# Kernel tuning notes

Hardware: AMD Instinct MI355X
Metric: run time of the kernel (lower is better)

Reference implementation:

```python
import jax, jax.numpy as jnp
import numpy as np

B, T, C_IN = 2, 4096, 1024
INTER, OUT = 1024, 1024
ROPE_DIM = 64
GAMMA = 0.99609375  # 1 - 2**-8
GROUPS = 32
EPS = 1e-6


def setup_inputs() -> dict:
    key = jax.random.key(0)
    k = jax.random.split(key, 4)
    return {
        "X_Q": jax.random.normal(k[0], (B, T, C_IN), dtype=jnp.float32),
        "W_Q": jax.random.normal(k[1], (C_IN, INTER), dtype=jnp.float32) / C_IN,
        "W_K": jax.random.normal(k[2], (C_IN, INTER), dtype=jnp.float32) / C_IN,
        "W_V": jax.random.normal(k[3], (C_IN, OUT), dtype=jnp.float32) / C_IN,
        "gn_weight": jnp.ones((OUT,), dtype=jnp.float32),
        "gn_bias": jnp.zeros((OUT,), dtype=jnp.float32),
    }


def _rope(x):
    # lucidrains RotaryEmbedding: rotate first ROPE_DIM features, pairwise-adjacent
    t = x.shape[-2]
    inv_freq = 1.0 / (10000.0 ** (jnp.arange(0, ROPE_DIM, 2, dtype=jnp.float32) / ROPE_DIM))
    freqs = jnp.arange(t, dtype=jnp.float32)[:, None] * inv_freq[None, :]  # [T, ROPE_DIM/2]
    freqs = jnp.repeat(freqs, 2, axis=-1)                                   # [T, ROPE_DIM]
    cos, sin = jnp.cos(freqs), jnp.sin(freqs)
    xr, xp = x[..., :ROPE_DIM], x[..., ROPE_DIM:]
    x1, x2 = xr[..., 0::2], xr[..., 1::2]
    rot = jnp.stack([-x2, x1], axis=-1).reshape(xr.shape)  # rotate_half (adjacent pairs)
    return jnp.concatenate([xr * cos + rot * sin, xp], axis=-1)


def _group_norm(x, w, b):
    # torch GroupNorm applied on x.reshape(-1, C)
    sh = x.shape
    c = sh[-1]
    xr = x.reshape(-1, GROUPS, c // GROUPS)
    mu = xr.mean(-1, keepdims=True)
    var = xr.var(-1, keepdims=True)
    xn = ((xr - mu) * jax.lax.rsqrt(var + EPS)).reshape(-1, c)
    return (xn * w + b).reshape(sh)


def reference(X_Q, W_Q, W_K, W_V, gn_weight, gn_bias):
    Q = jax.nn.silu(_rope(X_Q @ W_Q))  # [B,T,INTER]
    K = jax.nn.silu(_rope(X_Q @ W_K))
    V = jax.nn.silu(X_Q @ W_V)         # [B,T,OUT]
    A = jnp.einsum('btd,bsd->bts', Q, K)  # [B,T,T]
    # decay mask: original multiplies by _get_D(gamma,T).T -> gamma^(m-n) for m>=n
    n = jnp.arange(T)[:, None]
    m = jnp.arange(T)[None, :]
    upper = m >= n
    Dt = jnp.where(upper, GAMMA ** jnp.where(upper, m - n, 0).astype(jnp.float32), 0.0)
    A = A * Dt
    out = jnp.einsum('bts,bsd->btd', A, V)  # [B,T,OUT]
    # dropout p=0 (eval) -> identity
    return _group_norm(out, gn_weight, gn_bias)
```

## Files before the change

### kernel.cpp

```cpp
#include <hip/hip_runtime.h>


typedef __attribute__((ext_vector_type(8))) short bf16x8;
typedef __attribute__((ext_vector_type(4))) short bf16x4;
typedef __attribute__((ext_vector_type(4))) float f32x4;

#define MFMA16(a, b, c) __builtin_amdgcn_mfma_f32_16x16x32_bf16(a, b, c, 0, 0, 0)

static __device__ __forceinline__ short f2bf(float f) {
  unsigned u = __builtin_bit_cast(unsigned, f);
  u = (u + 0x7fffu + ((u >> 16) & 1u)) >> 16;
  return (short)u;
}

static __device__ __forceinline__ float fast_silu(float v) {
  return v * __builtin_amdgcn_rcpf(1.f + __expf(-v));
}

static __device__ __forceinline__ void gl_lds16(const void* g, void* l) {
  __builtin_amdgcn_global_load_lds(
      (const __attribute__((address_space(1))) void*)g,
      (__attribute__((address_space(3))) void*)l, 16, 0, 0);
}

static __device__ __forceinline__ int swzc(int col, int row) {
  return (((col >> 3) ^ (row & 7)) << 3) | (col & 7);
}

#define T_LEN 4096
#define CIN 1024

#define LOG2G (-0.0056465633f)
#define L2IF (0.41524101f)

__global__ __launch_bounds__(256)
void prep_kernel(const float* __restrict__ X, short* __restrict__ Xb,
                 const float* __restrict__ Wq, const float* __restrict__ Wk,
                 const float* __restrict__ Wv, short* __restrict__ WT) {
  __shared__ short tile[64][72];
  const int bx = blockIdx.x;
  const int tid = threadIdx.x;
  if (bx < 4096) {
    const int gid = bx * 256 + tid;
    const int row = gid >> 7;
    const int c = gid & 127;
    const float* s = &X[(size_t)gid * 8];
    float4 f0 = *(const float4*)s;
    float4 f1 = *(const float4*)(s + 4);
    bf16x8 v = {f2bf(f0.x), f2bf(f0.y), f2bf(f0.z), f2bf(f0.w),
                f2bf(f1.x), f2bf(f1.y), f2bf(f1.z), f2bf(f1.w)};
    const int pc = (c & 0x78) | ((c ^ row) & 7);
    *(bf16x8*)&Xb[(size_t)row * 1024 + pc * 8] = v;
    return;
  }
  const int bx2 = bx - 4096;
  const int k0 = (bx2 & 15) * 64, n0 = ((bx2 >> 4) & 15) * 64, mat = bx2 >> 8;
  const float* __restrict__ W = (mat == 0) ? Wq : (mat == 1) ? Wk : Wv;
  const int r = tid >> 4, c = tid & 15;
#pragma unroll
  for (int i = 0; i < 4; ++i) {
    int row = r + 16 * i;
    float4 f = *(const float4*)&W[(size_t)(k0 + row) * CIN + n0 + c * 4];
    tile[c * 4 + 0][row] = f2bf(f.x);
    tile[c * 4 + 1][row] = f2bf(f.y);
    tile[c * 4 + 2][row] = f2bf(f.z);
    tile[c * 4 + 3][row] = f2bf(f.w);
  }
  __syncthreads();
  const int n = tid >> 2, seg = tid & 3;
  bf16x8 lo = *(const bf16x8*)&tile[n][seg * 16];
  bf16x8 hi = *(const bf16x8*)&tile[n][seg * 16 + 8];
  const int R = mat * 1024 + n0 + n;
  const int a0 = (k0 >> 3) + seg * 2;
  short* base = &WT[(size_t)R * CIN];
  *(bf16x8*)&base[(a0 ^ (n & 7)) * 8] = lo;
  *(bf16x8*)&base[((a0 + 1) ^ (n & 7)) * 8] = hi;
}

#define GEMM_DECLS()                                   \
  const int tid = threadIdx.x;                         \
  const int lane = tid & 63, wave = tid >> 6;          \
  const int wm = wave >> 1, wn = wave & 1;             \
  const int l15 = lane & 15, quad = lane >> 4;         \
  const int srow = tid >> 3;                           \
  const int scol = (tid & 7) * 8;                      \
  const int asw = (l15 & 7);

#define ACC_INIT4(acc)                                 \
  _Pragma("unroll") for (int i = 0; i < 4; ++i)        \
  _Pragma("unroll") for (int j = 0; j < 4; ++j) {      \
    f32x4 z = {0.f, 0.f, 0.f, 0.f};                    \
    acc[i][j] = z;                                     \
  }

#define STAGE_TILE(dst, src, ld, r0, k0, nrows)        \
  _Pragma("unroll") for (int i = 0; i < (nrows) / 32; ++i) \
    gl_lds16(&src[(size_t)((r0) + i * 32 + srow) * (ld) + (k0) + scol], \
             &dst[i * 32 + srow][scol]);

#define FRAG_MFMA44(As, Bs, acc)                                            \
  {                                                                         \
    bf16x8 af[4][2], bfr[4][2];                                             \
    _Pragma("unroll") for (int im = 0; im < 4; ++im)                        \
    _Pragma("unroll") for (int ks = 0; ks < 2; ++ks)                        \
      af[im][ks] = *(const bf16x8*)&As[wm * 64 + im * 16 + l15]             \
                       [((ks * 4 + quad) ^ asw) * 8];                       \
    _Pragma("unroll") for (int in = 0; in < 4; ++in)                        \
    _Pragma("unroll") for (int ks = 0; ks < 2; ++ks)                        \
      bfr[in][ks] = *(const bf16x8*)&Bs[wn * 64 + in * 16 + l15]            \
                        [((ks * 4 + quad) ^ asw) * 8];                      \
    _Pragma("unroll") for (int ks = 0; ks < 2; ++ks)                        \
    _Pragma("unroll") for (int im = 0; im < 4; ++im)                        \
    _Pragma("unroll") for (int in = 0; in < 4; ++in)                        \
      acc[im][in] = MFMA16(af[im][ks], bfr[in][ks], acc[im][in]);           \
  }

__global__ __launch_bounds__(256, 2)
void qkv_gemm(const short* __restrict__ Xb, const short* __restrict__ WT,
              short* __restrict__ Qb, short* __restrict__ Kb,
              short* __restrict__ Vt) {
  __shared__ __align__(16) short As[128][64];
  __shared__ __align__(16) short Bs[128][64];
  GEMM_DECLS();
  const int m0 = blockIdx.x * 128;
  const int c0 = blockIdx.y * 128;

  f32x4 acc[4][4];
  ACC_INIT4(acc);

  for (int k0 = 0; k0 < CIN; k0 += 64) {
    __syncthreads();
    STAGE_TILE(As, Xb, CIN, m0, k0, 128);
    STAGE_TILE(Bs, WT, CIN, c0, k0, 128);
    __syncthreads();
    FRAG_MFMA44(As, Bs, acc);
  }

  const int mat = (c0 >> 10);
  const bool ropeBlk = (mat < 2) && ((c0 & 1023) == 0);
#pragma unroll
  for (int im = 0; im < 4; ++im) {
#pragma unroll
    for (int in = 0; in < 4; ++in) {
      const int c = c0 + wn * 64 + in * 16 + l15;
      const int colm = c & 1023;
      const int mbase = m0 + wm * 64 + im * 16 + quad * 4;
      short vv[4];
      if (ropeBlk && colm < 64) {
        const float invf = exp2f(-L2IF * (float)(colm >> 1));
#pragma unroll
        for (int r = 0; r < 4; ++r) {
          float v = acc[im][in][r];
          int t = (mbase + r) & (T_LEN - 1);
          float partner = __shfl_xor(v, 1, 64);
          float ang = (float)t * invf;
          float s_ = __sinf(ang), c_ = __cosf(ang);
          v = (colm & 1) ? (v * c_ + partner * s_) : (v * c_ - partner * s_);
          vv[r] = f2bf(fast_silu(v));
        }
      } else {
#pragma unroll
        for (int r = 0; r < 4; ++r) vv[r] = f2bf(fast_silu(acc[im][in][r]));
      }
      if (mat == 0) {
#pragma unroll
        for (int r = 0; r < 4; ++r)
          Qb[(size_t)(mbase + r) * 1024 + swzc(colm, mbase + r)] = vv[r];
      } else if (mat == 1) {
#pragma unroll
        for (int r = 0; r < 4; ++r)
          Kb[(size_t)(mbase + r) * 1024 + swzc(colm, mbase + r)] = vv[r];
      } else {
        bf16x4 v4 = {vv[0], vv[1], vv[2], vv[3]};
        *(bf16x4*)&Vt[(size_t)colm * 8192 +
                      (((mbase >> 3) ^ (colm & 7)) << 3) + (mbase & 7)] = v4;
      }
    }
  }
}

__global__ __launch_bounds__(256, 2)
void score_kernel(const short* __restrict__ Qb, const short* __restrict__ Kb,
                  short* __restrict__ Ab) {
  int idx = blockIdx.x;
  int ti = 0;
  while (idx >= 32 - ti) { idx -= 32 - ti; ++ti; }
  const int si = ti + idx;
  const int b = blockIdx.y;
  const int s0 = si * 128, t0 = ti * 128;

  __shared__ __align__(16) short Qs[128][64];
  __shared__ __align__(16) short Ks[128][64];
  GEMM_DECLS();

  f32x4 acc[4][4];
  ACC_INIT4(acc);

  for (int k0 = 0; k0 < 1024; k0 += 64) {
    __syncthreads();
    STAGE_TILE(Qs, Qb, 1024, b * T_LEN + t0, k0, 128);
    STAGE_TILE(Ks, Kb, 1024, b * T_LEN + s0, k0, 128);
    __syncthreads();
    FRAG_MFMA44(Qs, Ks, acc);
  }

#pragma unroll
  for (int im = 0; im < 4; ++im) {
#pragma unroll
    for (int in = 0; in < 4; ++in) {
      int s = s0 + wn * 64 + in * 16 + l15;
#pragma unroll
      for (int r = 0; r < 4; ++r) {
        int t = t0 + wm * 64 + im * 16 + quad * 4 + r;
        int d = s - t;
        float v = acc[im][in][r];
        v = (d < 0) ? 0.f : v * exp2f((float)d * LOG2G);
        Ab[((size_t)(b * T_LEN + t)) * T_LEN + swzc(s, t)] = f2bf(v);
      }
    }
  }
}

__global__ __launch_bounds__(256, 2)
void av_kernel(const short* __restrict__ Ab, const short* __restrict__ Vt,
               const float* __restrict__ gw, const float* __restrict__ gb,
               float* __restrict__ Out) {
  const int wgid = blockIdx.x;
  const int di = wgid & 7;
  const int q = (wgid >> 3) & 31;
  const int half = wgid >> 8;
  const int b = half;
  const int ti2 = half ? (31 - q) : q;
  const int t0 = ti2 * 128;
  const int n0 = di * 128;
  const int nIt = (T_LEN - t0) >> 6;

  __shared__ __align__(16) short As2[128][64];
  __shared__ __align__(16) short Vs[128][64];
  GEMM_DECLS();

  float w4[4], b4[4];
#pragma unroll
  for (int in = 0; in < 4; ++in) {
    int n = n0 + wn * 64 + in * 16 + l15;
    w4[in] = gw[n];
    b4[in] = gb[n];
  }

  f32x4 acc[4][4];
  ACC_INIT4(acc);

#pragma unroll 1
  for (int it = 0; it < nIt; ++it) {
    const int s = t0 + (it << 6);
    __syncthreads();
    STAGE_TILE(As2, Ab, T_LEN, b * T_LEN + t0, s, 128);
    STAGE_TILE(Vs, Vt, 8192, n0, b * T_LEN + s, 128);
    __syncthreads();
    FRAG_MFMA44(As2, Vs, acc);
  }

#pragma unroll
  for (int im = 0; im < 4; ++im) {
#pragma unroll
    for (int r = 0; r < 4; ++r) {
      int t = t0 + wm * 64 + im * 16 + quad * 4 + r;
      float* orow = &Out[((size_t)(b * T_LEN + t)) * 1024];
#pragma unroll
      for (int g = 0; g < 2; ++g) {
        float a0 = acc[im][g * 2][r], a1 = acc[im][g * 2 + 1][r];
        float s = a0 + a1;
        float qq = a0 * a0 + a1 * a1;
        s += __shfl_xor(s, 1, 64);
        qq += __shfl_xor(qq, 1, 64);
        s += __shfl_xor(s, 2, 64);
        qq += __shfl_xor(qq, 2, 64);
        s += __shfl_xor(s, 4, 64);
        qq += __shfl_xor(qq, 4, 64);
        s += __shfl_xor(s, 8, 64);
        qq += __shfl_xor(qq, 8, 64);
        float mean = s * (1.f / 32.f);
        float var = qq * (1.f / 32.f) - mean * mean;
        float rstd = rsqrtf(var + 1e-6f);
        int n = n0 + wn * 64 + g * 32 + l15;
        orow[n] = (a0 - mean) * rstd * w4[g * 2] + b4[g * 2];
        orow[n + 16] = (a1 - mean) * rstd * w4[g * 2 + 1] + b4[g * 2 + 1];
      }
    }
  }
}

extern "C" void kernel_launch(void* const* d_in, const int* in_sizes, int n_in,
                              void* d_out, int out_size, void* d_ws,
                              size_t ws_size, hipStream_t stream) {
  const float* X = (const float*)d_in[0];
  const float* Wq = (const float*)d_in[1];
  const float* Wk = (const float*)d_in[2];
  const float* Wv = (const float*)d_in[3];
  const float* gw = (const float*)d_in[4];
  const float* gb = (const float*)d_in[5];
  float* Out = (float*)d_out;

  short* Qb = (short*)d_ws;
  short* Kb = Qb + (size_t)8192 * 1024;
  short* Vt = Kb + (size_t)8192 * 1024;
  short* Ab = Vt + (size_t)8192 * 1024;
  short* Xb = Ab;
  short* WT = Xb + (size_t)8192 * 1024;

  prep_kernel<<<4864, 256, 0, stream>>>(X, Xb, Wq, Wk, Wv, WT);
  qkv_gemm<<<dim3(64, 24), 256, 0, stream>>>(Xb, WT, Qb, Kb, Vt);
  score_kernel<<<dim3(528, 2), 256, 0, stream>>>(Qb, Kb, Ab);
  av_kernel<<<512, 256, 0, stream>>>(Ab, Vt, gw, gb, Out);
}
```

Measured before the change: 280.9 us.

## Double-buffer QKV GEMM with async LDS prefetch and 256x128 tiles

The QKV projection GEMM now uses 512-thread blocks covering 256 rows by 128 columns, with two LDS buffers per operand. Direct global-to-LDS loads for the next K step are interleaved between MFMA phases, and s_setprio is raised around the MFMA bursts, replacing the old load-sync-compute loop. The aim is to hide global load latency behind matrix math and to reuse each B tile across more rows. In exchange LDS use doubles, there are more barriers per iteration, and the grid has half as many blocks, which may affect occupancy.

New measurement: 315.2 us. 1.12x slower.

```diff
diff --git a/kernel.cpp b/kernel.cpp
--- a/kernel.cpp
+++ b/kernel.cpp
@@ -115,26 +115,119 @@
       acc[im][in] = MFMA16(af[im][ks], bfr[in][ks], acc[im][in]);           \
   }
 
-__global__ __launch_bounds__(256, 2)
+__global__ __launch_bounds__(512, 2)
 void qkv_gemm(const short* __restrict__ Xb, const short* __restrict__ WT,
               short* __restrict__ Qb, short* __restrict__ Kb,
               short* __restrict__ Vt) {
-  __shared__ __align__(16) short As[128][64];
-  __shared__ __align__(16) short Bs[128][64];
-  GEMM_DECLS();
-  const int m0 = blockIdx.x * 128;
+  __shared__ __align__(16) short As[2][256][64];
+  __shared__ __align__(16) short Bs[2][128][64];
+  const int tid = threadIdx.x;
+  const int lane = tid & 63, wave = tid >> 6;
+  const int wm = wave >> 1, wn = wave & 1;
+  const int l15 = lane & 15, quad = lane >> 4;
+  const int srow = tid >> 3;
+  const int scol = (tid & 7) * 8;
+  const int asw = l15 & 7;
+  const int m0 = blockIdx.x * 256;
   const int c0 = blockIdx.y * 128;
 
   f32x4 acc[4][4];
   ACC_INIT4(acc);
 
-  for (int k0 = 0; k0 < CIN; k0 += 64) {
-    __syncthreads();
-    STAGE_TILE(As, Xb, CIN, m0, k0, 128);
-    STAGE_TILE(Bs, WT, CIN, c0, k0, 128);
-    __syncthreads();
-    FRAG_MFMA44(As, Bs, acc);
-  }
+#define QAF(dst, im, ks)                                                    \
+  dst = *(const bf16x8*)&As[cur][wm * 64 + (im)*16 + l15]                   \
+            [(((ks)*4 + quad) ^ asw) * 8];
+#define QBF(dst, in, ks)                                                    \
+  dst = *(const bf16x8*)&Bs[cur][wn * 64 + (in)*16 + l15]                   \
+            [(((ks)*4 + quad) ^ asw) * 8];
+#define QSA(buf, i, k0)                                                     \
+  gl_lds16(&Xb[(size_t)(m0 + (i)*64 + srow) * CIN + (k0) + scol],           \
+           &As[buf][(i)*64 + srow][scol]);
+#define QSB(buf, i, k0)                                                     \
+  gl_lds16(&WT[(size_t)(c0 + (i)*64 + srow) * CIN + (k0) + scol],           \
+           &Bs[buf][(i)*64 + srow][scol]);
+
+  QSA(0, 0, 0) QSA(0, 1, 0) QSA(0, 2, 0) QSA(0, 3, 0)
+  QSB(0, 0, 0) QSB(0, 1, 0)
+  asm volatile("s_waitcnt vmcnt(0)" ::: "memory");
+  __builtin_amdgcn_s_barrier();
+
+  int cur = 0;
+#pragma unroll 1
+  for (int t = 0; t < 16; ++t) {
+    const int nxt = cur ^ 1;
+    const int nk = (t + 1) << 6;
+    const bool pf = (t < 15);
+    bf16x8 a0f, a1f, b0f, b1f, b2f, b3f;
+
+    QAF(a0f, 0, 0) QAF(a1f, 1, 0)
+    QBF(b0f, 0, 0) QBF(b1f, 1, 0) QBF(b2f, 2, 0) QBF(b3f, 3, 0)
+    if (pf) { QSA(nxt, 0, nk) QSA(nxt, 1, nk) }
+    __builtin_amdgcn_s_barrier();
+    __builtin_amdgcn_s_setprio(1);
+    acc[0][0] = MFMA16(a0f, b0f, acc[0][0]);
+    acc[0][1] = MFMA16(a0f, b1f, acc[0][1]);
+    acc[0][2] = MFMA16(a0f, b2f, acc[0][2]);
+    acc[0][3] = MFMA16(a0f, b3f, acc[0][3]);
+    acc[1][0] = MFMA16(a1f, b0f, acc[1][0]);
+    acc[1][1] = MFMA16(a1f, b1f, acc[1][1]);
+    acc[1][2] = MFMA16(a1f, b2f, acc[1][2]);
+    acc[1][3] = MFMA16(a1f, b3f, acc[1][3]);
+    __builtin_amdgcn_s_setprio(0);
+    __builtin_amdgcn_s_barrier();
+
+    QAF(a0f, 2, 0) QAF(a1f, 3, 0)
+    if (pf) { QSA(nxt, 2, nk) QSA(nxt, 3, nk) }
+    __builtin_amdgcn_s_barrier();
+    __builtin_amdgcn_s_setprio(1);
+    acc[2][0] = MFMA16(a0f, b0f, acc[2][0]);
+    acc[2][1] = MFMA16(a0f, b1f, acc[2][1]);
+    acc[2][2] = MFMA16(a0f, b2f, acc[2][2]);
+    acc[2][3] = MFMA16(a0f, b3f, acc[2][3]);
+    acc[3][0] = MFMA16(a1f, b0f, acc[3][0]);
+    acc[3][1] = MFMA16(a1f, b1f, acc[3][1]);
+    acc[3][2] = MFMA16(a1f, b2f, acc[3][2]);
+    acc[3][3] = MFMA16(a1f, b3f, acc[3][3]);
+    __builtin_amdgcn_s_setprio(0);
+    __builtin_amdgcn_s_barrier();
+
+    QAF(a0f, 0, 1) QAF(a1f, 1, 1)
+    QBF(b0f, 0, 1) QBF(b1f, 1, 1) QBF(b2f, 2, 1) QBF(b3f, 3, 1)
+    if (pf) { QSB(nxt, 0, nk) }
+    __builtin_amdgcn_s_barrier();
+    __builtin_amdgcn_s_setprio(1);
+    acc[0][0] = MFMA16(a0f, b0f, acc[0][0]);
+    acc[0][1] = MFMA16(a0f, b1f, acc[0][1]);
+    acc[0][2] = MFMA16(a0f, b2f, acc[0][2]);
+    acc[0][3] = MFMA16(a0f, b3f, acc[0][3]);
+    acc[1][0] = MFMA16(a1f, b0f, acc[1][0]);
+    acc[1][1] = MFMA16(a1f, b1f, acc[1][1]);
+    acc[1][2] = MFMA16(a1f, b2f, acc[1][2]);
+    acc[1][3] = MFMA16(a1f, b3f, acc[1][3]);
+    __builtin_amdgcn_s_setprio(0);
+    __builtin_amdgcn_s_barrier();
+
+    QAF(a0f, 2, 1) QAF(a1f, 3, 1)
+    if (pf) { QSB(nxt, 1, nk) }
+    __builtin_amdgcn_s_barrier();
+    __builtin_amdgcn_s_setprio(1);
+    acc[2][0] = MFMA16(a0f, b0f, acc[2][0]);
+    acc[2][1] = MFMA16(a0f, b1f, acc[2][1]);
+    acc[2][2] = MFMA16(a0f, b2f, acc[2][2]);
+    acc[2][3] = MFMA16(a0f, b3f, acc[2][3]);
+    acc[3][0] = MFMA16(a1f, b0f, acc[3][0]);
+    acc[3][1] = MFMA16(a1f, b1f, acc[3][1]);
+    acc[3][2] = MFMA16(a1f, b2f, acc[3][2]);
+    acc[3][3] = MFMA16(a1f, b3f, acc[3][3]);
+    __builtin_amdgcn_s_setprio(0);
+    asm volatile("s_waitcnt vmcnt(0)" ::: "memory");
+    __builtin_amdgcn_s_barrier();
+    cur = nxt;
+  }
+#undef QAF
+#undef QBF
+#undef QSA
+#undef QSB
 
   const int mat = (c0 >> 10);
   const bool ropeBlk = (mat < 2) && ((c0 & 1023) == 0);
@@ -309,7 +402,7 @@
   short* WT = Xb + (size_t)8192 * 1024;
 
   prep_kernel<<<4864, 256, 0, stream>>>(X, Xb, Wq, Wk, Wv, WT);
-  qkv_gemm<<<dim3(64, 24), 256, 0, stream>>>(Xb, WT, Qb, Kb, Vt);
+  qkv_gemm<<<dim3(32, 24), 512, 0, stream>>>(Xb, WT, Qb, Kb, Vt);
   score_kernel<<<dim3(528, 2), 256, 0, stream>>>(Qb, Kb, Ab);
   av_kernel<<<512, 256, 0, stream>>>(Ab, Vt, gw, gb, Out);
 }
```
